# Optimization experiments

Measured on AMD Instinct MI355X. Metric: run time of the kernel, lower is better.

## Reference

```python
import jax, jax.numpy as jnp
import numpy as np

EPS = 1e-6
SCALE = 1.0
GRID_HEIGHT = 4.0
GRID_RES_Y = 1.0


def _perspective(mat, vec):
    # mat [3,4], vec [...,3] -> (points [...,2], flag [...,3])
    homog = jnp.einsum('ij,...j->...i', mat[:, :3], vec) + mat[:, 3]
    pos = homog[..., 2:3] > 0
    flag = jnp.concatenate([pos, pos, jnp.ones_like(pos)], axis=-1).astype(homog.dtype)
    homog = homog * flag  # zero x,y behind camera; z kept (flag[...,-1]=True)
    return homog[..., :2] / homog[..., 2:3], flag


def _fisheye(pts, k, D, flag):
    cx, cy, fx, fy = k[0, 2], k[1, 2], k[0, 0], k[1, 1]
    x = (pts[..., 0] - cx) / fx
    y = (pts[..., 1] - cy) / fy
    r = jnp.sqrt(x * x + y * y)
    th = jnp.arctan(r)
    t2 = th * th
    rad = th * (1 + D[0] * t2 + D[1] * t2 ** 2 + D[2] * t2 ** 3 + D[5] * t2 ** 4) / r
    xd = x * rad * fx + cx
    yd = y * rad * fy + cy
    return jnp.stack([xd, yd], axis=-1) * flag[..., :2]


def _pinhole(pts, k, D, flag):
    cx, cy, fx, fy = k[0, 2], k[1, 2], k[0, 0], k[1, 1]
    x = (pts[..., 0] - cx) / fx
    y = (pts[..., 1] - cy) / fy
    k1, k2, k3, p1, p2 = D[0], D[1], D[2], D[3], D[4]
    r2 = x * x + y * y
    poly = 1 + k1 * r2 + k2 * r2 * r2 + k3 * r2 * r2 * r2
    xd = x * poly + (2 * p1 * x * y + p2 * (r2 + 2 * x * x))
    yd = y * poly + (p1 * (r2 + 2 * y * y) + 2 * p2 * x * y)
    return jnp.stack([xd * fx + cx, yd * fy + cy], axis=-1) * flag[..., :2]


def _bilinear(img, coords):
    # torch F.grid_sample(align_corners=True, padding_mode='border'); img [C,H,W], coords [...,2] in [-1,1]
    C, H, W = img.shape
    x = jnp.clip((coords[..., 0] + 1) * 0.5 * (W - 1), 0.0, W - 1)
    y = jnp.clip((coords[..., 1] + 1) * 0.5 * (H - 1), 0.0, H - 1)
    x0 = jnp.floor(x)
    y0 = jnp.floor(y)
    wx = x - x0
    wy = y - y0
    x0i = x0.astype(jnp.int32)
    y0i = y0.astype(jnp.int32)
    x1i = jnp.minimum(x0i + 1, W - 1)
    y1i = jnp.minimum(y0i + 1, H - 1)
    flat = img.reshape(C, H * W)

    def g(yi, xi):
        return jnp.take(flat, (yi * W + xi).reshape(-1), axis=1).reshape((C,) + coords.shape[:-1])

    v00 = g(y0i, x0i)
    v01 = g(y0i, x1i)
    v10 = g(y1i, x0i)
    v11 = g(y1i, x1i)
    return v00 * (1 - wx) * (1 - wy) + v01 * wx * (1 - wy) + v10 * (1 - wx) * wy + v11 * wx * wy


def _per_image(feature, k, imu2c, post_rot, post_tran, undist, corner):
    C, Hf, Wf = feature.shape
    calib = k @ imu2c                                  # [3,4]
    pts, flag = _perspective(calib, corner)            # pts [Ny,Zd,Xd,2]
    pts = jnp.where(undist[-1] == 1,
                    _fisheye(pts, k, undist, flag),
                    _pinhole(pts, k, undist, flag))
    pts = jnp.einsum('ij,...j->...i', post_rot[:2, :2], pts) + post_tran[:2]
    nc = jnp.clip(2.0 * (pts / SCALE) - 1.0, -1.0, 1.0)  # [Ny,Zd,Xd,2]
    s0, s1 = slice(None, -1), slice(1, None)
    # 8 voxel corners -> [8, Ny-1, D, Wd, 2]
    corners8 = jnp.stack([nc[a, b, c] for a in (s0, s1) for b in (s0, s1) for c in (s0, s1)], axis=0)
    left = corners8[..., 0].min(0)
    right = corners8[..., 0].max(0)
    top = corners8[..., 1].min(0)
    bot = corners8[..., 1].max(0)
    Nh, D, Wd = left.shape
    bbox = jnp.stack([left, top, right, bot], axis=-1).reshape(Nh, D * Wd, 4)
    area = (bbox[..., 2] - bbox[..., 0]) * (bbox[..., 3] - bbox[..., 1]) * Hf * Wf * 0.25 + EPS  # [Nh,P]
    integ = jnp.cumsum(jnp.cumsum(feature, axis=-1), axis=-2)  # integral image [C,Hf,Wf]
    tl = _bilinear(integ, bbox[..., 0:2])
    br = _bilinear(integ, bbox[..., 2:4])
    tr = _bilinear(integ, jnp.stack([bbox[..., 2], bbox[..., 1]], axis=-1))
    bl = _bilinear(integ, jnp.stack([bbox[..., 0], bbox[..., 3]], axis=-1))
    vox = (tl + br - tr - bl) / area * (area > EPS)    # [C,Nh,P]
    return vox.reshape(C * Nh, D, Wd)                  # neck == '2d'


def _forward(features, ks, imu2cs, post_rots, post_trans, undists, grid):
    ys = -jnp.arange(0.0, GRID_HEIGHT, GRID_RES_Y) + GRID_HEIGHT / 2.0
    y_corners = jnp.stack([jnp.zeros_like(ys), ys, jnp.zeros_like(ys)], axis=-1)  # [Ny,3]
    corners = grid[:, None] + y_corners[None, :, None, None, :]                   # [B,Ny,Zd,Xd,3]
    per_cam = jax.vmap(_per_image, in_axes=(0, 0, 0, 0, 0, 0, None))

    def per_batch(f, k, m, pr, pt, ud, c):
        # drop_idx = [] -> all cameras kept; max over cameras
        return per_cam(f, k, m, pr, pt, ud, c).max(axis=0)

    return jax.vmap(per_batch)(features, ks, imu2cs, post_rots, post_trans, undists, corners)


def setup_inputs():
    key = jax.random.key(0)
    B, N, C, Hf, Wf = 1, 6, 64, 64, 176
    Zd = Xd = 129
    kf, ku = jax.random.split(key, 2)
    features = jax.random.normal(kf, (B, N, C, Hf, Wf), jnp.float32)
    # intrinsics (realistic pinhole values keep the projection numerically sane)
    K = np.zeros((B, N, 3, 3), np.float32)
    K[..., 0, 0] = 600.0
    K[..., 1, 1] = 600.0
    K[..., 0, 2] = 704.0
    K[..., 1, 2] = 256.0
    K[..., 2, 2] = 1.0
    ks = jnp.asarray(K)
    # extrinsics: per-camera yaw + small translation
    m = np.zeros((B, N, 3, 4), np.float32)
    for i in range(N):
        th = 0.25 * (i - 2.5)
        R = np.array([[np.cos(th), 0.0, np.sin(th)],
                      [0.0, 1.0, 0.0],
                      [-np.sin(th), 0.0, np.cos(th)]], np.float32)
        m[:, i, :, :3] = R
        m[:, i, :, 3] = np.array([0.1 * i, -1.5, 0.2], np.float32)
    imu2cs = jnp.asarray(m)
    pr = np.zeros((B, N, 3, 3), np.float32)
    pr[..., 0, 0] = 1.0 / 1408.0
    pr[..., 1, 1] = 1.0 / 512.0
    pr[..., 2, 2] = 1.0
    post_rots = jnp.asarray(pr)
    post_trans = jnp.zeros((B, N, 3), jnp.float32)
    und = 0.01 * np.array(jax.random.normal(ku, (B, N, 7)), np.float32)
    und[..., 6] = 0.0
    und[:, :3, 6] = 1.0  # first 3 cameras fisheye, rest pinhole
    undists = jnp.asarray(und)
    x = np.linspace(-40.0, 40.0, Xd, dtype=np.float32)
    z = np.linspace(3.0, 80.0, Zd, dtype=np.float32)
    zz, xx = np.meshgrid(z, x, indexing='ij')
    g = np.stack([xx, np.zeros_like(xx), zz], axis=-1)[None]  # [1,Zd,Xd,3]
    grid = jnp.asarray(np.broadcast_to(g, (B, Zd, Xd, 3)).copy())
    return {"features": features, "ks": ks, "imu2cs": imu2cs, "post_rots": post_rots,
            "post_trans": post_trans, "undists": undists, "grid": grid}


def reference(features, ks, imu2cs, post_rots, post_trans, undists, grid):
    return _forward(features, ks, imu2cs, post_rots, post_trans, undists, grid)
```

## Files before the change

kernel.cpp:

```cpp
#include <hip/hip_runtime.h>
#include <math.h>

#define NCAM 6
#define C_CH 64
#define HF   64
#define WF   176
#define GDIM 129
#define NY   4
#define NH   3
#define DD   128
#define WDIM 128
#define NP   (DD*WDIM)

struct alignas(16) BoxP {
    int   x0L, x0R, y0T, y0B;
    float wxL, wxR, wyT, wyB;
    float area; float pad0, pad1, pad2;
};
static_assert(sizeof(BoxP) == 48, "BoxP size");

__global__ void k_project(const float* __restrict__ ks,
                          const float* __restrict__ imu2cs,
                          const float* __restrict__ post_rots,
                          const float* __restrict__ post_trans,
                          const float* __restrict__ undists,
                          const float* __restrict__ grid,
                          float2* __restrict__ ncbuf)
{
    const int n   = blockIdx.y;
    const int idx = blockIdx.x * blockDim.x + threadIdx.x;
    const int per = NY * GDIM * GDIM;
    if (idx >= per) return;
    const int ny  = idx / (GDIM * GDIM);
    const int rem = idx % (GDIM * GDIM);
    const int gz  = rem / GDIM;
    const int gx  = rem % GDIM;

    const float* k  = ks         + n * 9;
    const float* m  = imu2cs     + n * 12;
    const float* pr = post_rots  + n * 9;
    const float* pt = post_trans + n * 3;
    const float* D  = undists    + n * 7;

    float cal[12];
    #pragma unroll
    for (int i = 0; i < 3; ++i)
        #pragma unroll
        for (int j = 0; j < 4; ++j)
            cal[i*4+j] = k[i*3+0]*m[0*4+j] + k[i*3+1]*m[1*4+j] + k[i*3+2]*m[2*4+j];

    const float vx = grid[(gz*GDIM + gx)*3 + 0];
    const float vy = 2.0f - (float)ny;
    const float vz = grid[(gz*GDIM + gx)*3 + 2];

    const float hx = cal[0]*vx + cal[1]*vy + cal[2]*vz  + cal[3];
    const float hy = cal[4]*vx + cal[5]*vy + cal[6]*vz  + cal[7];
    const float hz = cal[8]*vx + cal[9]*vy + cal[10]*vz + cal[11];

    const float fl = (hz > 0.0f) ? 1.0f : 0.0f;
    const float px = (hx * fl) / hz;
    const float py = (hy * fl) / hz;

    const float fx = k[0], fy = k[4], cx = k[2], cy = k[5];
    const float x = (px - cx) / fx;
    const float y = (py - cy) / fy;

    float xd, yd;
    if (D[6] == 1.0f) {
        const float r  = sqrtf(x*x + y*y);
        const float th = atanf(r);
        const float t2 = th * th;
        const float t4 = t2 * t2;
        const float rad = th * (1.0f + D[0]*t2 + D[1]*t4 + D[2]*(t2*t4) + D[5]*(t4*t4)) / r;
        xd = x * rad * fx + cx;
        yd = y * rad * fy + cy;
    } else {
        const float k1 = D[0], k2 = D[1], k3 = D[2], p1 = D[3], p2 = D[4];
        const float r2 = x*x + y*y;
        const float poly = 1.0f + k1*r2 + k2*r2*r2 + k3*r2*r2*r2;
        const float xdd = x*poly + (2.0f*p1*x*y + p2*(r2 + 2.0f*x*x));
        const float ydd = y*poly + (p1*(r2 + 2.0f*y*y) + 2.0f*p2*x*y);
        xd = xdd * fx + cx;
        yd = ydd * fy + cy;
    }
    xd *= fl; yd *= fl;

    const float qx = pr[0]*xd + pr[1]*yd + pt[0];
    const float qy = pr[3]*xd + pr[4]*yd + pt[1];
    const float ncx = fminf(fmaxf(2.0f*qx - 1.0f, -1.0f), 1.0f);
    const float ncy = fminf(fmaxf(2.0f*qy - 1.0f, -1.0f), 1.0f);
    ncbuf[((n*NY + ny)*GDIM + gz)*GDIM + gx] = make_float2(ncx, ncy);
}

__global__ __launch_bounds__(256) void k_rowcum(const float* __restrict__ feat,
                                                float* __restrict__ integ)
{
    __shared__ float lds[WF * 65];
    const int h   = blockIdx.x;
    const int n   = blockIdx.y;
    const int tid = threadIdx.x;

    for (int idx = tid; idx < C_CH * WF; idx += 256) {
        const int c = idx / WF;
        const int w = idx % WF;
        lds[w*65 + c] = feat[((size_t)(n*C_CH + c)*HF + h)*WF + w];
    }
    __syncthreads();
    if (tid < C_CH) {
        float run = 0.0f;
        for (int w = 0; w < WF; ++w) {
            run += lds[w*65 + tid];
            lds[w*65 + tid] = run;
        }
    }
    __syncthreads();
    float* outp = integ + (size_t)(n*HF + h) * (WF * C_CH);
    for (int idx = tid; idx < WF * C_CH; idx += 256) {
        const int w = idx / C_CH;
        const int c = idx % C_CH;
        outp[idx] = lds[w*65 + c];
    }
}

__global__ void k_colcum(float* __restrict__ integ)
{
    const int t = blockIdx.x * blockDim.x + threadIdx.x;
    const int n = blockIdx.y;
    if (t >= WF * C_CH) return;
    float* p = integ + (size_t)n * HF * WF * C_CH + t;
    float run = 0.0f;
    for (int h = 0; h < HF; ++h) {
        run += p[(size_t)h * (WF * C_CH)];
        p[(size_t)h * (WF * C_CH)] = run;
    }
}

__global__ void k_boxparams(const float2* __restrict__ ncbuf, BoxP* __restrict__ bp)
{
    const int idx = blockIdx.x * blockDim.x + threadIdx.x;
    if (idx >= NCAM * NH * NP) return;
    const int n  = idx / (NH * NP);
    const int r  = idx % (NH * NP);
    const int nh = r / NP;
    const int p  = r % NP;
    const int d  = p / WDIM;
    const int wd = p % WDIM;

    float left = 1e30f, right = -1e30f, top = 1e30f, bot = -1e30f;
    #pragma unroll
    for (int a = 0; a < 2; ++a)
        #pragma unroll
        for (int b = 0; b < 2; ++b)
            #pragma unroll
            for (int cc = 0; cc < 2; ++cc) {
                const float2 v = ncbuf[((n*NY + nh + a)*GDIM + d + b)*GDIM + wd + cc];
                left  = fminf(left,  v.x);  right = fmaxf(right, v.x);
                top   = fminf(top,   v.y);  bot   = fmaxf(bot,   v.y);
            }

    const float area = (right - left) * (bot - top) * (float)HF * (float)WF * 0.25f + 1e-6f;

    const float xLp = fminf(fmaxf((left  + 1.0f) * 0.5f * (float)(WF-1), 0.0f), (float)(WF-1));
    const float xRp = fminf(fmaxf((right + 1.0f) * 0.5f * (float)(WF-1), 0.0f), (float)(WF-1));
    const float yTp = fminf(fmaxf((top   + 1.0f) * 0.5f * (float)(HF-1), 0.0f), (float)(HF-1));
    const float yBp = fminf(fmaxf((bot   + 1.0f) * 0.5f * (float)(HF-1), 0.0f), (float)(HF-1));
    const float xL0 = floorf(xLp), xR0 = floorf(xRp), yT0 = floorf(yTp), yB0 = floorf(yBp);

    BoxP o;
    o.x0L = (int)xL0; o.x0R = (int)xR0; o.y0T = (int)yT0; o.y0B = (int)yB0;
    o.wxL = xLp - xL0; o.wxR = xRp - xR0; o.wyT = yTp - yT0; o.wyB = yBp - yB0;
    o.area = area; o.pad0 = 0.0f; o.pad1 = 0.0f; o.pad2 = 0.0f;
    bp[idx] = o;
}

__global__ __launch_bounds__(256) void k_sample(const float* __restrict__ integ,
                                                const BoxP* __restrict__ bp,
                                                float* __restrict__ out)
{
    __shared__ float sm[C_CH][17];
    const int nh   = blockIdx.y;
    const int p0   = blockIdx.x * 16;
    const int tid  = threadIdx.x;
    const int wave = tid >> 6;
    const int c    = tid & 63;

    #pragma unroll 1
    for (int j = 0; j < 4; ++j) {
        const int pj = p0 + wave*4 + j;
        float vmax = -3.402823466e38f;
        #pragma unroll 1
        for (int n = 0; n < NCAM; ++n) {
            const BoxP b = bp[(n*NH + nh)*NP + pj];
            const float* ib = integ + (size_t)n * (HF*WF*C_CH) + c;
            const int xL0 = b.x0L, xR0 = b.x0R, yT0 = b.y0T, yB0 = b.y0B;
            const int xL1 = min(xL0 + 1, WF-1), xR1 = min(xR0 + 1, WF-1);
            const int yT1 = min(yT0 + 1, HF-1), yB1 = min(yB0 + 1, HF-1);

            auto L = [&](int y, int x) -> float { return ib[(size_t)(y*WF + x) * C_CH]; };
            auto S = [&](int y0, int y1, float wy, int x0, int x1, float wx) -> float {
                const float v00 = L(y0, x0), v01 = L(y0, x1);
                const float v10 = L(y1, x0), v11 = L(y1, x1);
                return v00*(1.0f-wx)*(1.0f-wy) + v01*wx*(1.0f-wy)
                     + v10*(1.0f-wx)*wy        + v11*wx*wy;
            };
            const float tl = S(yT0, yT1, b.wyT, xL0, xL1, b.wxL);
            const float br = S(yB0, yB1, b.wyB, xR0, xR1, b.wxR);
            const float tr = S(yT0, yT1, b.wyT, xR0, xR1, b.wxR);
            const float bl = S(yB0, yB1, b.wyB, xL0, xL1, b.wxL);
            const float s  = tl + br - tr - bl;
            const float val = (b.area > 1e-6f) ? (s / b.area) : 0.0f;
            vmax = fmaxf(vmax, val);
        }
        sm[c][wave*4 + j] = vmax;
    }
    __syncthreads();
    for (int idx = tid; idx < C_CH * 16; idx += 256) {
        const int cc = idx >> 4;
        const int jj = idx & 15;
        out[(size_t)(cc*NH + nh)*NP + p0 + jj] = sm[cc][jj];
    }
}

extern "C" void kernel_launch(void* const* d_in, const int* in_sizes, int n_in,
                              void* d_out, int out_size, void* d_ws, size_t ws_size,
                              hipStream_t stream)
{
    const float* feats      = (const float*)d_in[0];
    const float* ks         = (const float*)d_in[1];
    const float* imu2cs     = (const float*)d_in[2];
    const float* post_rots  = (const float*)d_in[3];
    const float* post_trans = (const float*)d_in[4];
    const float* undists    = (const float*)d_in[5];
    const float* grid       = (const float*)d_in[6];
    float* out = (float*)d_out;

    char* ws = (char*)d_ws;
    size_t off = 0;
    float2* ncbuf = (float2*)(ws + off);
    off += sizeof(float2) * NCAM * NY * GDIM * GDIM;
    off = (off + 255) & ~(size_t)255;
    float* integ = (float*)(ws + off);
    off += sizeof(float) * NCAM * HF * WF * C_CH;
    off = (off + 255) & ~(size_t)255;
    BoxP* bp = (BoxP*)(ws + off);
    off += sizeof(BoxP) * NCAM * NH * NP;
    (void)ws_size; (void)in_sizes; (void)n_in; (void)out_size;

    dim3 g1((NY*GDIM*GDIM + 255)/256, NCAM);
    k_project<<<g1, 256, 0, stream>>>(ks, imu2cs, post_rots, post_trans, undists, grid, ncbuf);

    dim3 g2a(HF, NCAM);
    k_rowcum<<<g2a, 256, 0, stream>>>(feats, integ);

    dim3 g2b((WF*C_CH + 255)/256, NCAM);
    k_colcum<<<g2b, 256, 0, stream>>>(integ);

    dim3 g3((NCAM*NH*NP + 255)/256);
    k_boxparams<<<g3, 256, 0, stream>>>(ncbuf, bp);

    dim3 g4(NP/16, NH);
    k_sample<<<g4, 256, 0, stream>>>(integ, bp, out);
}
```

Measured before the change: 176.9 us.

## Precompute byte offsets, scalarize box params, parallelize row scan

The box-parameter kernel now stores precomputed byte row and column offsets, including the clamped +1 neighbours, in a 64-byte struct. The sampling kernel reads them uniformly through readfirstlane so they live in scalar registers. It also skips the loads for empty boxes, refactors the bilinear corner math into fmas, and uses an approximate reciprocal instead of a divide. The row cumulative sum is split into four segments scanned in parallel and then combined with segment offsets, and the column scan is unrolled. Using rcp slightly changes numerics, and the larger struct adds memory traffic.

```diff
diff --git a/kernel.cpp b/kernel.cpp
--- a/kernel.cpp
+++ b/kernel.cpp
@@ -12,12 +12,21 @@
 #define WDIM 128
 #define NP   (DD*WDIM)
 
-struct alignas(16) BoxP {
-    int   x0L, x0R, y0T, y0B;
+struct alignas(64) BoxP {
+    int   r0, r1, r2, r3;
+    int   c0, c1, c2, c3;
     float wxL, wxR, wyT, wyB;
-    float area; float pad0, pad1, pad2;
+    float area;
+    int   pad0, pad1, pad2;
 };
-static_assert(sizeof(BoxP) == 48, "BoxP size");
+static_assert(sizeof(BoxP) == 64, "BoxP size");
+
+__device__ __forceinline__ int rfl_i(int x) {
+    return __builtin_amdgcn_readfirstlane(x);
+}
+__device__ __forceinline__ float rfl_f(float x) {
+    return __builtin_bit_cast(float, __builtin_amdgcn_readfirstlane(__builtin_bit_cast(int, x)));
+}
 
 __global__ void k_project(const float* __restrict__ ks,
                           const float* __restrict__ imu2cs,
@@ -95,30 +104,45 @@
 __global__ __launch_bounds__(256) void k_rowcum(const float* __restrict__ feat,
                                                 float* __restrict__ integ)
 {
-    __shared__ float lds[WF * 65];
+    __shared__ float T[WF * 65];
+    __shared__ float S[4][C_CH];
+    __shared__ float OFF[4][C_CH];
     const int h   = blockIdx.x;
     const int n   = blockIdx.y;
     const int tid = threadIdx.x;
 
     for (int idx = tid; idx < C_CH * WF; idx += 256) {
-        const int c = idx / WF;
-        const int w = idx % WF;
-        lds[w*65 + c] = feat[((size_t)(n*C_CH + c)*HF + h)*WF + w];
+        const int cc = idx / WF;
+        const int w  = idx % WF;
+        T[w*65 + cc] = feat[((size_t)(n*C_CH + cc)*HF + h)*WF + w];
     }
     __syncthreads();
-    if (tid < C_CH) {
+    {
+        const int cc = tid & 63, seg = tid >> 6;
+        const int w0 = seg * 44;
         float run = 0.0f;
-        for (int w = 0; w < WF; ++w) {
-            run += lds[w*65 + tid];
-            lds[w*65 + tid] = run;
+        #pragma unroll
+        for (int i = 0; i < 44; ++i) {
+            run += T[(w0 + i)*65 + cc];
+            T[(w0 + i)*65 + cc] = run;
         }
+        S[seg][cc] = run;
+    }
+    __syncthreads();
+    {
+        const int cc = tid & 63, seg = tid >> 6;
+        float off = 0.0f;
+        #pragma unroll
+        for (int s = 0; s < 3; ++s)
+            if (s < seg) off += S[s][cc];
+        OFF[seg][cc] = off;
     }
     __syncthreads();
     float* outp = integ + (size_t)(n*HF + h) * (WF * C_CH);
     for (int idx = tid; idx < WF * C_CH; idx += 256) {
-        const int w = idx / C_CH;
-        const int c = idx % C_CH;
-        outp[idx] = lds[w*65 + c];
+        const int w  = idx >> 6;
+        const int cc = idx & 63;
+        outp[idx] = T[w*65 + cc] + OFF[w/44][cc];
     }
 }
 
@@ -129,6 +153,7 @@
     if (t >= WF * C_CH) return;
     float* p = integ + (size_t)n * HF * WF * C_CH + t;
     float run = 0.0f;
+    #pragma unroll
     for (int h = 0; h < HF; ++h) {
         run += p[(size_t)h * (WF * C_CH)];
         p[(size_t)h * (WF * C_CH)] = run;
@@ -166,10 +191,17 @@
     const float yBp = fminf(fmaxf((bot   + 1.0f) * 0.5f * (float)(HF-1), 0.0f), (float)(HF-1));
     const float xL0 = floorf(xLp), xR0 = floorf(xRp), yT0 = floorf(yTp), yB0 = floorf(yBp);
 
+    const int ixL0 = (int)xL0, ixR0 = (int)xR0, iyT0 = (int)yT0, iyB0 = (int)yB0;
+    const int ixL1 = min(ixL0 + 1, WF-1), ixR1 = min(ixR0 + 1, WF-1);
+    const int iyT1 = min(iyT0 + 1, HF-1), iyB1 = min(iyB0 + 1, HF-1);
+
     BoxP o;
-    o.x0L = (int)xL0; o.x0R = (int)xR0; o.y0T = (int)yT0; o.y0B = (int)yB0;
+    o.r0 = iyT0 * (WF*C_CH*4); o.r1 = iyT1 * (WF*C_CH*4);
+    o.r2 = iyB0 * (WF*C_CH*4); o.r3 = iyB1 * (WF*C_CH*4);
+    o.c0 = ixL0 * (C_CH*4);    o.c1 = ixL1 * (C_CH*4);
+    o.c2 = ixR0 * (C_CH*4);    o.c3 = ixR1 * (C_CH*4);
     o.wxL = xLp - xL0; o.wxR = xRp - xR0; o.wyT = yTp - yT0; o.wyB = yBp - yB0;
-    o.area = area; o.pad0 = 0.0f; o.pad1 = 0.0f; o.pad2 = 0.0f;
+    o.area = area; o.pad0 = 0; o.pad1 = 0; o.pad2 = 0;
     bp[idx] = o;
 }
 
@@ -181,7 +213,7 @@
     const int nh   = blockIdx.y;
     const int p0   = blockIdx.x * 16;
     const int tid  = threadIdx.x;
-    const int wave = tid >> 6;
+    const int wave = __builtin_amdgcn_readfirstlane(tid >> 6);
     const int c    = tid & 63;
 
     #pragma unroll 1
@@ -190,25 +222,40 @@
         float vmax = -3.402823466e38f;
         #pragma unroll 1
         for (int n = 0; n < NCAM; ++n) {
-            const BoxP b = bp[(n*NH + nh)*NP + pj];
-            const float* ib = integ + (size_t)n * (HF*WF*C_CH) + c;
-            const int xL0 = b.x0L, xR0 = b.x0R, yT0 = b.y0T, yB0 = b.y0B;
-            const int xL1 = min(xL0 + 1, WF-1), xR1 = min(xR0 + 1, WF-1);
-            const int yT1 = min(yT0 + 1, HF-1), yB1 = min(yB0 + 1, HF-1);
-
-            auto L = [&](int y, int x) -> float { return ib[(size_t)(y*WF + x) * C_CH]; };
-            auto S = [&](int y0, int y1, float wy, int x0, int x1, float wx) -> float {
-                const float v00 = L(y0, x0), v01 = L(y0, x1);
-                const float v10 = L(y1, x0), v11 = L(y1, x1);
-                return v00*(1.0f-wx)*(1.0f-wy) + v01*wx*(1.0f-wy)
-                     + v10*(1.0f-wx)*wy        + v11*wx*wy;
+            const BoxP* bpp = &bp[(n*NH + nh)*NP + pj];
+            const float area = rfl_f(bpp->area);
+            if (!(area > 1e-6f)) {
+                vmax = fmaxf(vmax, 0.0f);
+                continue;
+            }
+            const int r0 = rfl_i(bpp->r0), r1 = rfl_i(bpp->r1);
+            const int r2 = rfl_i(bpp->r2), r3 = rfl_i(bpp->r3);
+            const int c0 = rfl_i(bpp->c0), c1 = rfl_i(bpp->c1);
+            const int c2 = rfl_i(bpp->c2), c3 = rfl_i(bpp->c3);
+            const float wxL = rfl_f(bpp->wxL), wxR = rfl_f(bpp->wxR);
+            const float wyT = rfl_f(bpp->wyT), wyB = rfl_f(bpp->wyB);
+
+            const char* base = (const char*)integ + (size_t)n * (HF*WF*C_CH*4);
+            auto LD = [&](int ro, int co) -> float {
+                return ((const float*)(base + (size_t)(ro + co)))[c];
             };
-            const float tl = S(yT0, yT1, b.wyT, xL0, xL1, b.wxL);
-            const float br = S(yB0, yB1, b.wyB, xR0, xR1, b.wxR);
-            const float tr = S(yT0, yT1, b.wyT, xR0, xR1, b.wxR);
-            const float bl = S(yB0, yB1, b.wyB, xL0, xL1, b.wxL);
-            const float s  = tl + br - tr - bl;
-            const float val = (b.area > 1e-6f) ? (s / b.area) : 0.0f;
+            const float t0L0 = LD(r0,c0), t0L1 = LD(r0,c1), t0R0 = LD(r0,c2), t0R1 = LD(r0,c3);
+            const float t1L0 = LD(r1,c0), t1L1 = LD(r1,c1), t1R0 = LD(r1,c2), t1R1 = LD(r1,c3);
+            const float b0L0 = LD(r2,c0), b0L1 = LD(r2,c1), b0R0 = LD(r2,c2), b0R1 = LD(r2,c3);
+            const float b1L0 = LD(r3,c0), b1L1 = LD(r3,c1), b1R0 = LD(r3,c2), b1R1 = LD(r3,c3);
+
+            const float A0 = fmaf(wxL, t0L1 - t0L0, t0L0);
+            const float B0 = fmaf(wxR, t0R1 - t0R0, t0R0);
+            const float A1 = fmaf(wxL, t1L1 - t1L0, t1L0);
+            const float B1 = fmaf(wxR, t1R1 - t1R0, t1R0);
+            const float A2 = fmaf(wxL, b0L1 - b0L0, b0L0);
+            const float B2 = fmaf(wxR, b0R1 - b0R0, b0R0);
+            const float A3 = fmaf(wxL, b1L1 - b1L0, b1L0);
+            const float B3 = fmaf(wxR, b1R1 - b1R0, b1R0);
+            const float d0 = A0 - B0, d1 = A1 - B1;
+            const float e0 = B2 - A2, e1 = B3 - A3;
+            const float s = fmaf(wyT, d1 - d0, d0) + fmaf(wyB, e1 - e0, e0);
+            const float val = s * __builtin_amdgcn_rcpf(area);
             vmax = fmaxf(vmax, val);
         }
         sm[c][wave*4 + j] = vmax;
```

Result: faster. 161.0 us (-9.0%).
